# Kernel tuning notes

Measured on AMD Instinct MI355X. Metric: run time of the kernel, lower is better.

The kernel has to match this reference:

```python
import jax, jax.numpy as jnp
import numpy as np

N = 50000          # num_nodes
E = 500000         # num_edges
EMB = 50           # embedding_dim
HID = 64           # hidden_dim (per head, conv1)
OUT = 50           # out_dim (conv2, heads=1)
EDIM = 28          # edge_feature_dim
H = 4              # heads (conv1)
NEG_SLOPE = 0.2    # GATv2 leaky_relu slope
EPS_SM = 1e-16     # PyG softmax eps
EPS_LN = 1e-5      # PyG LayerNorm eps


def setup_inputs() -> dict:
    key = jax.random.key(0)
    ks = jax.random.split(key, 24)
    rn = lambda k, shape, s=0.1: jax.random.normal(k, shape, jnp.float32) * s
    return {
        "x": jax.random.randint(ks[0], (N,), 0, N),
        "edge_index": jax.random.randint(ks[1], (2, E), 0, N),
        "edge_attr": rn(ks[2], (E, EDIM), 1.0),
        "emb": rn(ks[3], (N, EMB), 1.0),
        # conv1 (GATv2Conv: lin_l/lin_r with bias, lin_edge no bias, att [H,C], out bias)
        "Wl1": rn(ks[4], (EMB, H * HID)), "bl1": jnp.zeros((H * HID,), jnp.float32),
        "Wr1": rn(ks[5], (EMB, H * HID)), "br1": jnp.zeros((H * HID,), jnp.float32),
        "We1": rn(ks[6], (EDIM, H * HID)),
        "att1": rn(ks[7], (H, HID)),
        "bias1": jnp.zeros((H * HID,), jnp.float32),
        "ln1_w": jnp.ones((H * HID,), jnp.float32), "ln1_b": jnp.zeros((H * HID,), jnp.float32),
        # conv2 (heads=1)
        "Wl2": rn(ks[8], (H * HID, OUT)), "bl2": jnp.zeros((OUT,), jnp.float32),
        "Wr2": rn(ks[9], (H * HID, OUT)), "br2": jnp.zeros((OUT,), jnp.float32),
        "We2": rn(ks[10], (EDIM, OUT)),
        "att2": rn(ks[11], (1, OUT)),
        "bias2": jnp.zeros((OUT,), jnp.float32),
        "ln2_w": jnp.ones((OUT,), jnp.float32), "ln2_b": jnp.zeros((OUT,), jnp.float32),
    }


def gatv2(h, src, dst, ea, Wl, bl, Wr, br, We, att, bias, heads, C):
    n = h.shape[0]
    xl = (h @ Wl + bl).reshape(n, heads, C)   # source transform [N,H,C]
    xr = (h @ Wr + br).reshape(n, heads, C)   # dest transform   [N,H,C]
    xe = (ea @ We).reshape(-1, heads, C)      # edge transform   [E,H,C]
    m = jax.nn.leaky_relu(xl[src] + xr[dst] + xe, NEG_SLOPE)  # [E,H,C]
    logits = jnp.einsum('ehc,hc->eh', m, att)                  # [E,H]
    # edge-softmax over incoming edges of each destination node
    amax = jax.ops.segment_max(logits, dst, num_segments=n)    # [N,H]
    ex = jnp.exp(logits - amax[dst])
    denom = jax.ops.segment_sum(ex, dst, num_segments=n)
    alpha = ex / (denom[dst] + EPS_SM)                         # [E,H]
    out = jax.ops.segment_sum(xl[src] * alpha[..., None], dst, num_segments=n)  # [N,H,C]
    return out.reshape(n, heads * C) + bias


def graph_layernorm(x, w, b):
    # PyG LayerNorm (default mode='graph', batch=None): scalar mean/std over whole tensor
    xc = x - x.mean()
    return xc / (xc.std() + EPS_LN) * w + b


def reference(x, edge_index, edge_attr, emb,
              Wl1, bl1, Wr1, br1, We1, att1, bias1, ln1_w, ln1_b,
              Wl2, bl2, Wr2, br2, We2, att2, bias2, ln2_w, ln2_b):
    src, dst = edge_index[0], edge_index[1]
    h = emb[x]                                                  # [N,EMB]
    h = gatv2(h, src, dst, edge_attr, Wl1, bl1, Wr1, br1, We1, att1, bias1, H, HID)
    h = jax.nn.relu(graph_layernorm(h, ln1_w, ln1_b))
    # dropout p=0.5 is identity in eval mode
    h = gatv2(h, src, dst, edge_attr, Wl2, bl2, Wr2, br2, We2, att2, bias2, 1, OUT)
    return graph_layernorm(h, ln2_w, ln2_b)
```

## Files before the change

kernel.cpp:

```cpp
#include <hip/hip_runtime.h>

#define N_NODES 50000
#define N_EDGES 500000
#define EMB 50
#define HID 64
#define OUTD 50
#define EDIM 28
#define HEADS 4
#define F1 256
#define NEG 0.2f
#define EPS_SM 1e-16f
#define EPS_LN 1e-5f
#define LOG2E 1.4426950408889634f

typedef unsigned short u16;
typedef unsigned int u32;
typedef _Float16 hf;
typedef hf h2 __attribute__((ext_vector_type(2)));
typedef hf hf8 __attribute__((ext_vector_type(8)));
typedef float f4 __attribute__((ext_vector_type(4)));
typedef short s8v __attribute__((ext_vector_type(8)));

__device__ __forceinline__ float b2f(u16 u) { return __uint_as_float(((u32)u) << 16); }
__device__ __forceinline__ u16 f2b(float f) {
    u32 u = __float_as_uint(f);
    u32 r = (u + 0x7FFFu + ((u >> 16) & 1u)) >> 16;
    return (u16)r;
}
__device__ __forceinline__ h2 uq(u32 u) { return __builtin_bit_cast(h2, u); }
__device__ __forceinline__ u32 hpack(float a, float b) {
    h2 p = {(hf)a, (hf)b};
    return __builtin_bit_cast(u32, p);
}
__device__ __forceinline__ float lrelu(float x) { return x > 0.f ? x : NEG * x; }

__global__ void k_init(int* __restrict__ cnt, int* __restrict__ cursor, float* __restrict__ S,
                       const float* __restrict__ a, u32* __restrict__ o,
                       const float* __restrict__ We1, const float* __restrict__ We2,
                       u32* __restrict__ Weh1, u32* __restrict__ Weh2,
                       const float* __restrict__ att1, const float* __restrict__ att2,
                       float* __restrict__ atts1, float* __restrict__ atts2,
                       const float* __restrict__ emb, u16* __restrict__ embb) {
    int i = blockIdx.x * blockDim.x + threadIdx.x;
    if (i < N_NODES) cnt[i] = 0;
    else if (i < 2 * N_NODES) cursor[i - N_NODES] = 0;
    else if (i < 2 * N_NODES + 4) S[i - 2 * N_NODES] = 0.f;
    if (i < F1 * 16) {
        int k2 = i >> 8, c = i & 255;
        Weh1[i] = (k2 < 14) ? hpack(We1[(2 * k2) * F1 + c], We1[(2 * k2 + 1) * F1 + c]) : 0u;
    } else if (i < F1 * 16 + 64 * 16) {
        int j = i - F1 * 16;
        int k2 = j >> 6, c = j & 63;
        Weh2[j] = (k2 < 14 && c < OUTD) ? hpack(We2[(2 * k2) * OUTD + c], We2[(2 * k2 + 1) * OUTD + c]) : 0u;
    } else {
        int ja = i - (F1 * 16 + 64 * 16);
        if (ja < 256) atts1[ja] = att1[ja] * LOG2E;
        else if (ja < 320) {
            int c = ja - 256;
            atts2[c] = (c < OUTD) ? att2[c] * LOG2E : 0.f;
        }
    }
    if (i < N_NODES * 64) {
        int node = i >> 6, k = i & 63;
        embb[i] = (k < EMB) ? f2b(emb[(size_t)node * EMB + k]) : (u16)0;
    }
    if (i < N_EDGES * 8) {
        int e = i >> 3, part = i & 7;
        if (part < 7) {
            float4 v = *(const float4*)(a + (size_t)e * EDIM + part * 4);
            *(uint2*)(o + (size_t)e * 16 + part * 2) = make_uint2(hpack(v.x, v.y), hpack(v.z, v.w));
        } else {
            *(uint2*)(o + (size_t)e * 16 + 14) = make_uint2(0u, 0u);
        }
    }
}

__global__ void k_packw(const float* __restrict__ Wl1, const float* __restrict__ Wr1,
                        u16* __restrict__ Wlt1, u16* __restrict__ Wrt1,
                        const float* __restrict__ Wl2, const float* __restrict__ Wr2,
                        u16* __restrict__ Wlt2, u16* __restrict__ Wrt2) {
    int i = blockIdx.x * blockDim.x + threadIdx.x;
    if (i < 256 * 64) {
        int c = i >> 6, k = i & 63;
        Wlt1[i] = (k < EMB) ? f2b(Wl1[k * F1 + c]) : (u16)0;
        Wrt1[i] = (k < EMB) ? f2b(Wr1[k * F1 + c]) : (u16)0;
    } else if (i < 2 * 256 * 64) {
        int j = i - 256 * 64;
        int c = j >> 8, k = j & 255;
        Wlt2[j] = (c < OUTD) ? f2b(Wl2[k * OUTD + c]) : (u16)0;
        Wrt2[j] = (c < OUTD) ? f2b(Wr2[k * OUTD + c]) : (u16)0;
    }
}

__global__ void k_hist(const int* __restrict__ dst, int* __restrict__ cnt) {
    int e = blockIdx.x * blockDim.x + threadIdx.x;
    if (e < N_EDGES) atomicAdd(&cnt[dst[e]], 1);
}

__global__ __launch_bounds__(1024) void k_scan(const int* __restrict__ cnt, int* __restrict__ rowptr) {
    __shared__ int part[1024];
    int tid = threadIdx.x;
    const int CH = (N_NODES + 1023) / 1024;
    int beg = tid * CH;
    int end = beg + CH; if (end > N_NODES) end = N_NODES;
    int s = 0;
    for (int i = beg; i < end && i >= beg; i++) s += cnt[i];
    part[tid] = s;
    __syncthreads();
    for (int off = 1; off < 1024; off <<= 1) {
        int v = (tid >= off) ? part[tid - off] : 0;
        __syncthreads();
        part[tid] += v;
        __syncthreads();
    }
    int run = (tid == 0) ? 0 : part[tid - 1];
    for (int i = beg; i < end && i >= beg; i++) { rowptr[i] = run; run += cnt[i]; }
    if (tid == 1023) rowptr[N_NODES] = run;
}

__global__ void k_scatter(const int* __restrict__ src, const int* __restrict__ dst,
                          const int* __restrict__ rowptr, int* __restrict__ cursor,
                          int2* __restrict__ epk, int* __restrict__ dstc) {
    int e = blockIdx.x * blockDim.x + threadIdx.x;
    if (e >= N_EDGES) return;
    int d = dst[e];
    int pos = atomicAdd(&cursor[d], 1);
    int j = rowptr[d] + pos;
    epk[j] = make_int2(e << 6, src[e]);
    dstc[j] = d;
}

__global__ __launch_bounds__(256) void k_sumpart(const float* __restrict__ P, int n, float* __restrict__ S) {
    float s1 = 0.f, s2 = 0.f;
    int stride = gridDim.x * blockDim.x;
    for (int i = blockIdx.x * blockDim.x + threadIdx.x; i < n; i += stride) {
        s1 += P[2 * i]; s2 += P[2 * i + 1];
    }
    #pragma unroll
    for (int off = 32; off; off >>= 1) { s1 += __shfl_xor(s1, off); s2 += __shfl_xor(s2, off); }
    __shared__ float w1[4], w2[4];
    int w = threadIdx.x >> 6;
    if ((threadIdx.x & 63) == 0) { w1[w] = s1; w2[w] = s2; }
    __syncthreads();
    if (threadIdx.x == 0) {
        atomicAdd(S,     w1[0] + w1[1] + w1[2] + w1[3]);
        atomicAdd(S + 1, w2[0] + w2[1] + w2[2] + w2[3]);
    }
}

__global__ __launch_bounds__(256) void k_node1(
    const int* __restrict__ x, const u16* __restrict__ embb,
    const u16* __restrict__ Wlt, const u16* __restrict__ Wrt,
    const float* __restrict__ bl, const float* __restrict__ br,
    u16* __restrict__ xl, u16* __restrict__ xr)
{
    int w = threadIdx.x >> 6, lane = threadIdx.x & 63;
    int c = lane & 15, kg = lane >> 4;
    s8v bL[4][2], bR[4][2];
    float blv[4], brv[4];
    #pragma unroll
    for (int ct = 0; ct < 4; ct++) {
        int col = (w << 6) + (ct << 4) + c;
        #pragma unroll
        for (int ks = 0; ks < 2; ks++) {
            bL[ct][ks] = *(const s8v*)(Wlt + ((u32)col << 6) + (ks << 5) + (kg << 3));
            bR[ct][ks] = *(const s8v*)(Wrt + ((u32)col << 6) + (ks << 5) + (kg << 3));
        }
        blv[ct] = bl[col];
        brv[ct] = br[col];
    }
    const int NTILES = N_NODES / 16;
    for (int t = blockIdx.x; t < NTILES; t += gridDim.x) {
        int nb = t << 4;
        int xi = x[nb + c];
        const u16* er = embb + ((u32)xi << 6);
        s8v a0 = *(const s8v*)(er + (kg << 3));
        s8v a1 = *(const s8v*)(er + 32 + (kg << 3));
        #pragma unroll
        for (int ct = 0; ct < 4; ct++) {
            int col = (w << 6) + (ct << 4) + c;
            f4 accL = {blv[ct], blv[ct], blv[ct], blv[ct]};
            f4 accR = {brv[ct], brv[ct], brv[ct], brv[ct]};
            accL = __builtin_amdgcn_mfma_f32_16x16x32_bf16(a0, bL[ct][0], accL, 0, 0, 0);
            accL = __builtin_amdgcn_mfma_f32_16x16x32_bf16(a1, bL[ct][1], accL, 0, 0, 0);
            accR = __builtin_amdgcn_mfma_f32_16x16x32_bf16(a0, bR[ct][0], accR, 0, 0, 0);
            accR = __builtin_amdgcn_mfma_f32_16x16x32_bf16(a1, bR[ct][1], accR, 0, 0, 0);
            #pragma unroll
            for (int i = 0; i < 4; i++) {
                int node = nb + (kg << 2) + i;
                xl[((size_t)node << 8) + col] = f2b(accL[i]);
                xr[((size_t)node << 8) + col] = f2b(accR[i]);
            }
        }
    }
}

__global__ __launch_bounds__(256) void k_logits1(
    const int2* __restrict__ epk, const int* __restrict__ dstc,
    const u32* __restrict__ eah, const u16* __restrict__ xl, const u16* __restrict__ xr,
    const u32* __restrict__ Weh, const float* __restrict__ atts,
    float* __restrict__ Lg)
{
    int lane = threadIdx.x & 63;
    int er = lane & 15, grp = lane >> 4;
    hf8 wA[16];
    #pragma unroll
    for (int ct = 0; ct < 16; ct++) {
        uint4 q;
        q.x = Weh[(grp * 4 + 0) * 256 + ct * 16 + er];
        q.y = Weh[(grp * 4 + 1) * 256 + ct * 16 + er];
        q.z = Weh[(grp * 4 + 2) * 256 + ct * 16 + er];
        q.w = Weh[(grp * 4 + 3) * 256 + ct * 16 + er];
        wA[ct] = __builtin_bit_cast(hf8, q);
    }
    int wid = blockIdx.x * 4 + (threadIdx.x >> 6);
    int nw = gridDim.x * 4;
    const int NT = N_EDGES / 16;
    const char* eab = (const char*)eah;
    const f4 zero = {0.f, 0.f, 0.f, 0.f};
    if (wid >= NT) return;
    int2 p = epk[wid * 16 + er];
    int d = dstc[wid * 16 + er];
    for (int t = wid; t < NT; t += nw) {
        int tn = t + nw;
        int2 pn; int dn;
        if (tn < NT) { pn = epk[tn * 16 + er]; dn = dstc[tn * 16 + er]; }
        int j = t * 16 + er;
        hf8 bfrag = *(const hf8*)(eab + (u32)p.x + (grp << 4));
        const u16* xlp = xl + ((u32)p.y << 8);
        const u16* xrp = xr + ((u32)d << 8);
        float part0 = 0.f, part1 = 0.f, part2 = 0.f, part3 = 0.f;
        #pragma unroll
        for (int ct = 0; ct < 16; ct++) {
            int c0 = ct * 16 + grp * 4;
            f4 z = __builtin_amdgcn_mfma_f32_16x16x32_f16(wA[ct], bfrag, zero, 0, 0, 0);
            uint2 ql = *(const uint2*)(xlp + c0);
            uint2 qr = *(const uint2*)(xrp + c0);
            float4 av = *(const float4*)(atts + c0);
            float z0 = z[0] + __uint_as_float(ql.x << 16)        + __uint_as_float(qr.x << 16);
            float z1 = z[1] + __uint_as_float(ql.x & 0xFFFF0000u) + __uint_as_float(qr.x & 0xFFFF0000u);
            float z2 = z[2] + __uint_as_float(ql.y << 16)        + __uint_as_float(qr.y << 16);
            float z3 = z[3] + __uint_as_float(ql.y & 0xFFFF0000u) + __uint_as_float(qr.y & 0xFFFF0000u);
            float s = av.x * fmaxf(z0, NEG * z0) + av.y * fmaxf(z1, NEG * z1)
                    + av.z * fmaxf(z2, NEG * z2) + av.w * fmaxf(z3, NEG * z3);
            if      (ct < 4)  part0 += s;
            else if (ct < 8)  part1 += s;
            else if (ct < 12) part2 += s;
            else              part3 += s;
        }
        part0 += __shfl_xor(part0, 16); part0 += __shfl_xor(part0, 32);
        part1 += __shfl_xor(part1, 16); part1 += __shfl_xor(part1, 32);
        part2 += __shfl_xor(part2, 16); part2 += __shfl_xor(part2, 32);
        part3 += __shfl_xor(part3, 16); part3 += __shfl_xor(part3, 32);
        float v01 = (grp & 1) ? part1 : part0;
        float v23 = (grp & 1) ? part3 : part2;
        float v = (grp & 2) ? v23 : v01;
        Lg[((size_t)j << 2) + grp] = v;
        p = pn; d = dn;
    }
}

__global__ __launch_bounds__(256) void k_fused1(
    const int* __restrict__ rowptr, const int2* __restrict__ epk,
    const float* __restrict__ Lg, const u16* __restrict__ xl,
    const float* __restrict__ bias, u16* __restrict__ out, float* __restrict__ Spart)
{
    int node = blockIdx.x;
    int tid = threadIdx.x;
    int h = tid >> 6, lane = tid & 63;
    int beg = rowptr[node], end = rowptr[node + 1];
    float acc = 0.f, dtot = 0.f;
    int j = beg;
    for (; j + 3 < end; j += 4) {
        int2 pA = epk[j], pB = epk[j + 1], pC = epk[j + 2], pD = epk[j + 3];
        float g1 = Lg[((size_t)j << 2) + h];
        float g2 = Lg[((size_t)j << 2) + 4 + h];
        float g3 = Lg[((size_t)j << 2) + 8 + h];
        float g4 = Lg[((size_t)j << 2) + 12 + h];
        float xA = b2f(xl[((u32)pA.y << 8) + tid]);
        float xB = b2f(xl[((u32)pB.y << 8) + tid]);
        float xC = b2f(xl[((u32)pC.y << 8) + tid]);
        float xD = b2f(xl[((u32)pD.y << 8) + tid]);
        float p1 = exp2f(g1), p2 = exp2f(g2), p3 = exp2f(g3), p4 = exp2f(g4);
        acc  += (p1 * xA + p2 * xB) + (p3 * xC + p4 * xD);
        dtot += (p1 + p2) + (p3 + p4);
    }
    for (; j < end; j++) {
        int2 p = epk[j];
        float pe = exp2f(Lg[((size_t)j << 2) + h]);
        float xA = b2f(xl[((u32)p.y << 8) + tid]);
        acc += pe * xA; dtot += pe;
    }
    float o = ((end > beg) ? acc / (dtot + EPS_SM) : 0.f) + bias[tid];
    out[((size_t)node << 8) + tid] = f2b(o);
    float s1 = o, s2 = o * o;
    #pragma unroll
    for (int off = 32; off; off >>= 1) { s1 += __shfl_xor(s1, off); s2 += __shfl_xor(s2, off); }
    __shared__ float ls1[4], ls2[4];
    if (lane == 0) { ls1[h] = s1; ls2[h] = s2; }
    __syncthreads();
    if (tid == 0) {
        Spart[(size_t)node * 2]     = ls1[0] + ls1[1] + ls1[2] + ls1[3];
        Spart[(size_t)node * 2 + 1] = ls2[0] + ls2[1] + ls2[2] + ls2[3];
    }
}

__global__ void k_ln_apply_relu_b(
    u16* v, const float* __restrict__ w, const float* __restrict__ b,
    const float* __restrict__ S, int M, int C)
{
    int i = blockIdx.x * blockDim.x + threadIdx.x;
    if (i >= M) return;
    float mu = S[0] / (float)M;
    float var = S[1] / (float)M - mu * mu;
    float inv = 1.f / (sqrtf(fmaxf(var, 0.f)) + EPS_LN);
    int c = i % C;
    float y = (b2f(v[i]) - mu) * inv * w[c] + b[c];
    v[i] = f2b(fmaxf(y, 0.f));
}

__global__ void k_ln_out(
    const float* __restrict__ v, const float* __restrict__ w, const float* __restrict__ b,
    const float* __restrict__ S, int M, int C, float* __restrict__ out)
{
    int i = blockIdx.x * blockDim.x + threadIdx.x;
    if (i >= M) return;
    float mu = S[0] / (float)M;
    float var = S[1] / (float)M - mu * mu;
    float inv = 1.f / (sqrtf(fmaxf(var, 0.f)) + EPS_LN);
    int c = i % C;
    out[i] = (v[i] - mu) * inv * w[c] + b[c];
}

__global__ __launch_bounds__(256) void k_node2(
    const u16* __restrict__ h, const u16* __restrict__ Wlt, const u16* __restrict__ Wrt,
    const float* __restrict__ bl, const float* __restrict__ br,
    u16* __restrict__ xlb, u16* __restrict__ xrb)
{
    int w = threadIdx.x >> 6, lane = threadIdx.x & 63;
    int c = lane & 15, kg = lane >> 4;
    int col = (w << 4) + c;
    s8v bL[8], bR[8];
    #pragma unroll
    for (int ks = 0; ks < 8; ks++) {
        bL[ks] = *(const s8v*)(Wlt + ((u32)col << 8) + (ks << 5) + (kg << 3));
        bR[ks] = *(const s8v*)(Wrt + ((u32)col << 8) + (ks << 5) + (kg << 3));
    }
    float blv = (col < OUTD) ? bl[col] : 0.f;
    float brv = (col < OUTD) ? br[col] : 0.f;
    const int NTILES = N_NODES / 16;
    for (int t = blockIdx.x; t < NTILES; t += gridDim.x) {
        int nb = t << 4;
        const u16* hrow = h + ((size_t)(nb + c) << 8) + (kg << 3);
        f4 accL = {blv, blv, blv, blv};
        f4 accR = {brv, brv, brv, brv};
        #pragma unroll
        for (int ks = 0; ks < 8; ks++) {
            s8v a = *(const s8v*)(hrow + (ks << 5));
            accL = __builtin_amdgcn_mfma_f32_16x16x32_bf16(a, bL[ks], accL, 0, 0, 0);
            accR = __builtin_amdgcn_mfma_f32_16x16x32_bf16(a, bR[ks], accR, 0, 0, 0);
        }
        #pragma unroll
        for (int i = 0; i < 4; i++) {
            int node = nb + (kg << 2) + i;
            xlb[((u32)node << 6) + col] = f2b(accL[i]);
            xrb[((u32)node << 6) + col] = f2b(accR[i]);
        }
    }
}

__global__ __launch_bounds__(256) void k_logits2(
    const int2* __restrict__ epk, const int* __restrict__ dstc,
    const u32* __restrict__ eah, const u16* __restrict__ xlb, const u16* __restrict__ xrb,
    const u32* __restrict__ Weh, const float* __restrict__ atts,
    float* __restrict__ Lg2)
{
    int lane = threadIdx.x & 63;
    int er = lane & 15, grp = lane >> 4;
    hf8 wA[4];
    #pragma unroll
    for (int ct = 0; ct < 4; ct++) {
        uint4 q;
        q.x = Weh[(grp * 4 + 0) * 64 + ct * 16 + er];
        q.y = Weh[(grp * 4 + 1) * 64 + ct * 16 + er];
        q.z = Weh[(grp * 4 + 2) * 64 + ct * 16 + er];
        q.w = Weh[(grp * 4 + 3) * 64 + ct * 16 + er];
        wA[ct] = __builtin_bit_cast(hf8, q);
    }
    int wid = blockIdx.x * 4 + (threadIdx.x >> 6);
    int nw = gridDim.x * 4;
    const int NT = N_EDGES / 16;
    const char* eab = (const char*)eah;
    const f4 zero = {0.f, 0.f, 0.f, 0.f};
    if (wid >= NT) return;
    int2 p = epk[wid * 16 + er];
    int d = dstc[wid * 16 + er];
    for (int t = wid; t < NT; t += nw) {
        int tn = t + nw;
        int2 pn; int dn;
        if (tn < NT) { pn = epk[tn * 16 + er]; dn = dstc[tn * 16 + er]; }
        int j = t * 16 + er;
        hf8 bfrag = *(const hf8*)(eab + (u32)p.x + (grp << 4));
        const u16* xlp = xlb + ((u32)p.y << 6);
        const u16* xrp = xrb + ((u32)d << 6);
        float tot = 0.f;
        #pragma unroll
        for (int ct = 0; ct < 4; ct++) {
            int c0 = ct * 16 + grp * 4;
            f4 z = __builtin_amdgcn_mfma_f32_16x16x32_f16(wA[ct], bfrag, zero, 0, 0, 0);
            uint2 ql = *(const uint2*)(xlp + c0);
            uint2 qr = *(const uint2*)(xrp + c0);
            float4 av = *(const float4*)(atts + c0);
            float z0 = z[0] + __uint_as_float(ql.x << 16)        + __uint_as_float(qr.x << 16);
            float z1 = z[1] + __uint_as_float(ql.x & 0xFFFF0000u) + __uint_as_float(qr.x & 0xFFFF0000u);
            float z2 = z[2] + __uint_as_float(ql.y << 16)        + __uint_as_float(qr.y << 16);
            float z3 = z[3] + __uint_as_float(ql.y & 0xFFFF0000u) + __uint_as_float(qr.y & 0xFFFF0000u);
            tot += av.x * fmaxf(z0, NEG * z0) + av.y * fmaxf(z1, NEG * z1)
                 + av.z * fmaxf(z2, NEG * z2) + av.w * fmaxf(z3, NEG * z3);
        }
        tot += __shfl_xor(tot, 16);
        tot += __shfl_xor(tot, 32);
        if (lane < 16) Lg2[j] = tot;
        p = pn; d = dn;
    }
}

__global__ __launch_bounds__(256) void k_fused2(
    const int* __restrict__ rowptr, const int2* __restrict__ epk,
    const float* __restrict__ Lg2, const u16* __restrict__ xlb,
    const float* __restrict__ bias, float* __restrict__ out, float* __restrict__ Spart)
{
    int w = threadIdx.x >> 6, lane = threadIdx.x & 63;
    int node = blockIdx.x * 4 + w;
    bool col = lane < OUTD;
    int beg = rowptr[node], end = rowptr[node + 1];
    float acc = 0.f, dtot = 0.f;
    int j = beg;
    for (; j + 3 < end; j += 4) {
        int2 p0 = epk[j], p1 = epk[j + 1], p2 = epk[j + 2], p3 = epk[j + 3];
        float g0 = Lg2[j], g1 = Lg2[j + 1], g2 = Lg2[j + 2], g3 = Lg2[j + 3];
        float x0 = b2f(xlb[((u32)p0.y << 6) + lane]);
        float x1 = b2f(xlb[((u32)p1.y << 6) + lane]);
        float x2 = b2f(xlb[((u32)p2.y << 6) + lane]);
        float x3 = b2f(xlb[((u32)p3.y << 6) + lane]);
        float e0 = exp2f(g0), e1 = exp2f(g1), e2 = exp2f(g2), e3 = exp2f(g3);
        acc  += (e0 * x0 + e1 * x1) + (e2 * x2 + e3 * x3);
        dtot += (e0 + e1) + (e2 + e3);
    }
    for (; j < end; j++) {
        int2 p = epk[j];
        float e = exp2f(Lg2[j]);
        float xv = b2f(xlb[((u32)p.y << 6) + lane]);
        acc += e * xv; dtot += e;
    }
    float s1 = 0.f, s2 = 0.f;
    if (col) {
        float o = ((end > beg) ? acc / (dtot + EPS_SM) : 0.f) + bias[lane];
        out[(u32)node * OUTD + lane] = o;
        s1 = o; s2 = o * o;
    }
    #pragma unroll
    for (int off = 32; off; off >>= 1) { s1 += __shfl_xor(s1, off); s2 += __shfl_xor(s2, off); }
    __shared__ float ls1[4], ls2[4];
    if (lane == 0) { ls1[w] = s1; ls2[w] = s2; }
    __syncthreads();
    if (threadIdx.x == 0) {
        Spart[(size_t)blockIdx.x * 2]     = ls1[0] + ls1[1] + ls1[2] + ls1[3];
        Spart[(size_t)blockIdx.x * 2 + 1] = ls2[0] + ls2[1] + ls2[2] + ls2[3];
    }
}

extern "C" void kernel_launch(void* const* d_in, const int* in_sizes, int n_in,
                              void* d_out, int out_size, void* d_ws, size_t ws_size,
                              hipStream_t stream)
{
    const int*   x    = (const int*)d_in[0];
    const int*   ei   = (const int*)d_in[1];
    const int*   srcA = ei;
    const int*   dstA = ei + N_EDGES;
    const float* ea   = (const float*)d_in[2];
    const float* emb  = (const float*)d_in[3];
    const float* Wl1  = (const float*)d_in[4];
    const float* bl1  = (const float*)d_in[5];
    const float* Wr1  = (const float*)d_in[6];
    const float* br1  = (const float*)d_in[7];
    const float* We1  = (const float*)d_in[8];
    const float* att1 = (const float*)d_in[9];
    const float* bias1= (const float*)d_in[10];
    const float* ln1w = (const float*)d_in[11];
    const float* ln1b = (const float*)d_in[12];
    const float* Wl2  = (const float*)d_in[13];
    const float* bl2  = (const float*)d_in[14];
    const float* Wr2  = (const float*)d_in[15];
    const float* br2  = (const float*)d_in[16];
    const float* We2  = (const float*)d_in[17];
    const float* att2 = (const float*)d_in[18];
    const float* bias2= (const float*)d_in[19];
    const float* ln2w = (const float*)d_in[20];
    const float* ln2b = (const float*)d_in[21];

    float* W = (float*)d_ws;
    u16*   xl1b    = (u16*)W;
    u16*   xr1b    = (u16*)(W + 6400000);
    u16*   out1b   = (u16*)(W + 12800000);
    u32*   eah     = (u32*)(W + 19200000);
    int2*  epk     = (int2*)(W + 27200000);
    int*   rowptr  = (int*)(W + 28200000);
    int*   cnt     = (int*)(W + 28260000);
    int*   cursor  = (int*)(W + 28310000);
    float* Spart   = W + 28360000;
    float* S       = W + 28460000;
    u32*   Weh1    = (u32*)(W + 28470000);
    u32*   Weh2    = (u32*)(W + 28480000);
    float* atts1   = W + 28481100;
    float* atts2   = W + 28481600;
    int*   dstc    = (int*)(W + 28482000);
    u16*   Wlt2    = (u16*)(W + 28982000);
    u16*   Wrt2    = (u16*)(W + 28991000);
    float* Lg      = W + 29000000;
    u16*   embb    = (u16*)(W + 29000000);
    u16*   Wlt1    = (u16*)(W + 30600000);
    u16*   Wrt1    = (u16*)(W + 30610000);
    u16*   xl2b    = (u16*)W;
    u16*   xr2b    = (u16*)(W + 1600000);
    float* out2    = W + 3200000;
    float* Lg2     = W + 29000000;
    u16*   h1      = out1b;

    k_init<<<(N_EDGES * 8 + 255) / 256, 256, 0, stream>>>(cnt, cursor, S, ea, eah,
                                                          We1, We2, Weh1, Weh2,
                                                          att1, att2, atts1, atts2,
                                                          emb, embb);
    k_packw<<<128, 256, 0, stream>>>(Wl1, Wr1, Wlt1, Wrt1, Wl2, Wr2, Wlt2, Wrt2);
    k_hist<<<(N_EDGES + 255) / 256, 256, 0, stream>>>(dstA, cnt);
    k_scan<<<1, 1024, 0, stream>>>(cnt, rowptr);
    k_scatter<<<(N_EDGES + 255) / 256, 256, 0, stream>>>(srcA, dstA, rowptr, cursor, epk, dstc);

    k_node1<<<1024, 256, 0, stream>>>(x, embb, Wlt1, Wrt1, bl1, br1, xl1b, xr1b);
    k_logits1<<<1024, 256, 0, stream>>>(epk, dstc, eah, xl1b, xr1b, Weh1, atts1, Lg);
    k_fused1<<<N_NODES, 256, 0, stream>>>(rowptr, epk, Lg, xl1b, bias1, out1b, Spart);
    k_sumpart<<<32, 256, 0, stream>>>(Spart, N_NODES, S);
    k_ln_apply_relu_b<<<(N_NODES * F1 + 255) / 256, 256, 0, stream>>>(h1, ln1w, ln1b, S, N_NODES * F1, F1);

    k_node2<<<1024, 256, 0, stream>>>(h1, Wlt2, Wrt2, bl2, br2, xl2b, xr2b);
    k_logits2<<<1024, 256, 0, stream>>>(epk, dstc, eah, xl2b, xr2b, Weh2, atts2, Lg2);
    k_fused2<<<N_NODES / 4, 256, 0, stream>>>(rowptr, epk, Lg2, xl2b, bias2, out2, Spart);
    k_sumpart<<<32, 256, 0, stream>>>(Spart, N_NODES / 4, S + 2);
    k_ln_out<<<(N_NODES * OUTD + 255) / 256, 256, 0, stream>>>(out2, ln2w, ln2b, S + 2, N_NODES * OUTD, OUTD, (float*)d_out);
}
```

Before: 590.3 us.

## Parallelize CSR scan across blocks and prefetch edge-feature fragments

```diff
diff --git a/kernel.cpp b/kernel.cpp
--- a/kernel.cpp
+++ b/kernel.cpp
@@ -12,6 +12,7 @@
 #define EPS_SM 1e-16f
 #define EPS_LN 1e-5f
 #define LOG2E 1.4426950408889634f
+#define SCAN_B 196
 
 typedef unsigned short u16;
 typedef unsigned int u32;
@@ -97,25 +98,50 @@
     if (e < N_EDGES) atomicAdd(&cnt[dst[e]], 1);
 }
 
-__global__ __launch_bounds__(1024) void k_scan(const int* __restrict__ cnt, int* __restrict__ rowptr) {
-    __shared__ int part[1024];
+__global__ __launch_bounds__(256) void k_scan1(const int* __restrict__ cnt, int* __restrict__ bsum) {
+    int i = blockIdx.x * 256 + threadIdx.x;
+    int v = (i < N_NODES) ? cnt[i] : 0;
+    #pragma unroll
+    for (int off = 32; off; off >>= 1) v += __shfl_xor(v, off);
+    __shared__ int ws[4];
+    if ((threadIdx.x & 63) == 0) ws[threadIdx.x >> 6] = v;
+    __syncthreads();
+    if (threadIdx.x == 0) bsum[blockIdx.x] = ws[0] + ws[1] + ws[2] + ws[3];
+}
+
+__global__ __launch_bounds__(256) void k_scan2(int* __restrict__ bsum) {
+    __shared__ int lds[256];
     int tid = threadIdx.x;
-    const int CH = (N_NODES + 1023) / 1024;
-    int beg = tid * CH;
-    int end = beg + CH; if (end > N_NODES) end = N_NODES;
-    int s = 0;
-    for (int i = beg; i < end && i >= beg; i++) s += cnt[i];
-    part[tid] = s;
+    int v = (tid < SCAN_B) ? bsum[tid] : 0;
+    lds[tid] = v;
     __syncthreads();
-    for (int off = 1; off < 1024; off <<= 1) {
-        int v = (tid >= off) ? part[tid - off] : 0;
+    for (int off = 1; off < 256; off <<= 1) {
+        int t = (tid >= off) ? lds[tid - off] : 0;
         __syncthreads();
-        part[tid] += v;
+        lds[tid] += t;
         __syncthreads();
     }
-    int run = (tid == 0) ? 0 : part[tid - 1];
-    for (int i = beg; i < end && i >= beg; i++) { rowptr[i] = run; run += cnt[i]; }
-    if (tid == 1023) rowptr[N_NODES] = run;
+    if (tid < SCAN_B) bsum[tid] = lds[tid] - v;
+}
+
+__global__ __launch_bounds__(256) void k_scan3(const int* __restrict__ cnt, const int* __restrict__ bsum,
+                                               int* __restrict__ rowptr) {
+    __shared__ int lds[256];
+    int tid = threadIdx.x;
+    int i = blockIdx.x * 256 + tid;
+    int v = (i < N_NODES) ? cnt[i] : 0;
+    lds[tid] = v;
+    __syncthreads();
+    for (int off = 1; off < 256; off <<= 1) {
+        int t = (tid >= off) ? lds[tid - off] : 0;
+        __syncthreads();
+        lds[tid] += t;
+        __syncthreads();
+    }
+    int incl = lds[tid];
+    int base = bsum[blockIdx.x];
+    if (i < N_NODES) rowptr[i] = base + incl - v;
+    if (i == N_NODES - 1) rowptr[N_NODES] = base + incl;
 }
 
 __global__ void k_scatter(const int* __restrict__ src, const int* __restrict__ dst,
@@ -221,12 +247,16 @@
     if (wid >= NT) return;
     int2 p = epk[wid * 16 + er];
     int d = dstc[wid * 16 + er];
+    hf8 bfrag = *(const hf8*)(eab + (u32)p.x + (grp << 4));
     for (int t = wid; t < NT; t += nw) {
         int tn = t + nw;
-        int2 pn; int dn;
-        if (tn < NT) { pn = epk[tn * 16 + er]; dn = dstc[tn * 16 + er]; }
+        int2 pn; int dn; hf8 bfn;
+        if (tn < NT) {
+            pn = epk[tn * 16 + er];
+            dn = dstc[tn * 16 + er];
+            bfn = *(const hf8*)(eab + (u32)pn.x + (grp << 4));
+        }
         int j = t * 16 + er;
-        hf8 bfrag = *(const hf8*)(eab + (u32)p.x + (grp << 4));
         const u16* xlp = xl + ((u32)p.y << 8);
         const u16* xrp = xr + ((u32)d << 8);
         float part0 = 0.f, part1 = 0.f, part2 = 0.f, part3 = 0.f;
@@ -256,7 +286,7 @@
         float v23 = (grp & 1) ? part3 : part2;
         float v = (grp & 2) ? v23 : v01;
         Lg[((size_t)j << 2) + grp] = v;
-        p = pn; d = dn;
+        p = pn; d = dn; bfrag = bfn;
     }
 }
 
@@ -395,12 +425,16 @@
     if (wid >= NT) return;
     int2 p = epk[wid * 16 + er];
     int d = dstc[wid * 16 + er];
+    hf8 bfrag = *(const hf8*)(eab + (u32)p.x + (grp << 4));
     for (int t = wid; t < NT; t += nw) {
         int tn = t + nw;
-        int2 pn; int dn;
-        if (tn < NT) { pn = epk[tn * 16 + er]; dn = dstc[tn * 16 + er]; }
+        int2 pn; int dn; hf8 bfn;
+        if (tn < NT) {
+            pn = epk[tn * 16 + er];
+            dn = dstc[tn * 16 + er];
+            bfn = *(const hf8*)(eab + (u32)pn.x + (grp << 4));
+        }
         int j = t * 16 + er;
-        hf8 bfrag = *(const hf8*)(eab + (u32)p.x + (grp << 4));
         const u16* xlp = xlb + ((u32)p.y << 6);
         const u16* xrp = xrb + ((u32)d << 6);
         float tot = 0.f;
@@ -421,7 +455,7 @@
         tot += __shfl_xor(tot, 16);
         tot += __shfl_xor(tot, 32);
         if (lane < 16) Lg2[j] = tot;
-        p = pn; d = dn;
+        p = pn; d = dn; bfrag = bfn;
     }
 }
 
@@ -510,6 +544,7 @@
     int*   cursor  = (int*)(W + 28310000);
     float* Spart   = W + 28360000;
     float* S       = W + 28460000;
+    int*   bsum    = (int*)(W + 28461000);
     u32*   Weh1    = (u32*)(W + 28470000);
     u32*   Weh2    = (u32*)(W + 28480000);
     float* atts1   = W + 28481100;
@@ -533,7 +568,9 @@
                                                           emb, embb);
     k_packw<<<128, 256, 0, stream>>>(Wl1, Wr1, Wlt1, Wrt1, Wl2, Wr2, Wlt2, Wrt2);
     k_hist<<<(N_EDGES + 255) / 256, 256, 0, stream>>>(dstA, cnt);
-    k_scan<<<1, 1024, 0, stream>>>(cnt, rowptr);
+    k_scan1<<<SCAN_B, 256, 0, stream>>>(cnt, bsum);
+    k_scan2<<<1, 256, 0, stream>>>(bsum);
+    k_scan3<<<SCAN_B, 256, 0, stream>>>(cnt, bsum, rowptr);
     k_scatter<<<(N_EDGES + 255) / 256, 256, 0, stream>>>(srcA, dstA, rowptr, cursor, epk, dstc);
 
     k_node1<<<1024, 256, 0, stream>>>(x, embb, Wlt1, Wrt1, bl1, br1, xl1b, xr1b);
```

New measurement: 526.2 us. -10.9%, faster.
